# Performance work log

Measured on AMD Instinct MI355X. Metric: run time of the kernel, lower is better.

The kernel has to match this reference:

```python
import jax, jax.numpy as jnp
import numpy as np

B, S, I, H = 32, 1024, 512, 512


def setup_inputs() -> dict:
    key = jax.random.key(0)
    ks = jax.random.split(key, 5)
    scale_ih = 1.0 / np.sqrt(I)
    scale_hh = 1.0 / np.sqrt(H)
    return {
        "x": jax.random.normal(ks[0], (B, S, I), dtype=jnp.float32),
        "W_ih": jax.random.normal(ks[1], (4 * H, I), dtype=jnp.float32) * scale_ih,
        "W_hh": jax.random.normal(ks[2], (4 * H, H), dtype=jnp.float32) * scale_hh,
        "b_ih": jax.random.normal(ks[3], (4 * H,), dtype=jnp.float32) * scale_hh,
        "b_hh": jax.random.normal(ks[4], (4 * H,), dtype=jnp.float32) * scale_hh,
        "h0": jnp.zeros((B, H), dtype=jnp.float32),
        "c0": jnp.zeros((B, H), dtype=jnp.float32),
    }


def reference(x, W_ih, W_hh, b_ih, b_hh, h0, c0):
    # Precompute input contribution for all timesteps: [B, S, 4H]
    x_gates = jnp.einsum('bsi,gi->bsg', x, W_ih) + b_ih + b_hh

    def step(carry, xg_t):
        h, c = carry
        gates = xg_t + h @ W_hh.T  # [B, 4H]
        i_g, f_g, g_g, o_g = jnp.split(gates, 4, axis=-1)
        i_g = jax.nn.sigmoid(i_g)
        f_g = jax.nn.sigmoid(f_g)
        g_g = jnp.tanh(g_g)
        o_g = jax.nn.sigmoid(o_g)
        c_new = f_g * c + i_g * g_g
        h_new = o_g * jnp.tanh(c_new)
        return (h_new, c_new), h_new

    # scan over time: [S, B, 4H]
    (h_n, c_n), ys = jax.lax.scan(step, (h0, c0), jnp.swapaxes(x_gates, 0, 1))
    output = jnp.swapaxes(ys, 0, 1)  # [B, S, H]
    return output, h_n, c_n
```

## Files before the change

### kernel.cpp

```cpp
#include <hip/hip_runtime.h>
#include <stdint.h>


typedef __attribute__((ext_vector_type(8))) short bf16x8;
typedef __attribute__((ext_vector_type(4))) float f32x4;

__device__ __forceinline__ unsigned short f2bf(float f) {
  union { float f; unsigned u; } v; v.f = f;
  unsigned r = (v.u + 0x7fffu + ((v.u >> 16) & 1u)) >> 16;
  return (unsigned short)r;
}
__device__ __forceinline__ float bf2f(unsigned short h) {
  union { unsigned u; float f; } v; v.u = ((unsigned)h) << 16;
  return v.f;
}

__global__ __launch_bounds__(256) void cvt_bf16(const float* __restrict__ in,
                                                unsigned short* __restrict__ out, int n) {
  int i = (blockIdx.x * 256 + threadIdx.x) * 4;
  if (i >= n) return;
  float4 v = *(const float4*)(in + i);
  ushort4 o;
  o.x = f2bf(v.x); o.y = f2bf(v.y); o.z = f2bf(v.z); o.w = f2bf(v.w);
  *(ushort4*)(out + i) = o;
}

__global__ __launch_bounds__(256) void gemm_xg(const unsigned short* __restrict__ A,
                                               const unsigned short* __restrict__ Bw,
                                               const float* __restrict__ b_ih,
                                               const float* __restrict__ b_hh,
                                               unsigned short* __restrict__ xg) {
  __shared__ unsigned short Asub[128][32];
  __shared__ unsigned short Bsub[128][32];
  const int tid = threadIdx.x;
  const int mb = blockIdx.x >> 4;
  const int nb = blockIdx.x & 15;
  const int wv = tid >> 6, ln = tid & 63;
  const int wr = wv >> 1, wc = wv & 1;
  const int lrow = tid >> 1;
  const int lseg = (tid & 1) * 16;

  const unsigned short* Ag = A + (size_t)(mb * 128 + lrow) * 512 + lseg;
  const unsigned short* Bg = Bw + (size_t)(nb * 128 + lrow) * 512 + lseg;

  f32x4 acc[4][4] = {};
  const int frow = ln & 15;
  const int kq = (ln >> 4) * 8;

  for (int k0 = 0; k0 < 512; k0 += 32) {
    uint4 a0 = *(const uint4*)(Ag + k0);
    uint4 a1 = *(const uint4*)(Ag + k0 + 8);
    uint4 b0 = *(const uint4*)(Bg + k0);
    uint4 b1 = *(const uint4*)(Bg + k0 + 8);
    __syncthreads();
    *(uint4*)&Asub[lrow][lseg]     = a0;
    *(uint4*)&Asub[lrow][lseg + 8] = a1;
    *(uint4*)&Bsub[lrow][lseg]     = b0;
    *(uint4*)&Bsub[lrow][lseg + 8] = b1;
    __syncthreads();
    bf16x8 af[4], bfr[4];
#pragma unroll
    for (int mi = 0; mi < 4; ++mi)
      af[mi] = *(const bf16x8*)&Asub[wr * 64 + mi * 16 + frow][kq];
#pragma unroll
    for (int ni = 0; ni < 4; ++ni)
      bfr[ni] = *(const bf16x8*)&Bsub[wc * 64 + ni * 16 + frow][kq];
#pragma unroll
    for (int mi = 0; mi < 4; ++mi)
#pragma unroll
      for (int ni = 0; ni < 4; ++ni)
        acc[mi][ni] = __builtin_amdgcn_mfma_f32_16x16x32_bf16(af[mi], bfr[ni], acc[mi][ni], 0, 0, 0);
  }

  const int col0 = nb * 128 + wc * 64 + frow;
  float bias[4];
#pragma unroll
  for (int ni = 0; ni < 4; ++ni)
    bias[ni] = b_ih[col0 + ni * 16] + b_hh[col0 + ni * 16];

#pragma unroll
  for (int mi = 0; mi < 4; ++mi) {
    const int m0 = mb * 128 + wr * 64 + mi * 16 + (ln >> 4) * 4;
#pragma unroll
    for (int ni = 0; ni < 4; ++ni) {
#pragma unroll
      for (int rr = 0; rr < 4; ++rr) {
        float v = acc[mi][ni][rr] + bias[ni];
        xg[(size_t)(m0 + rr) * 2048 + col0 + ni * 16] = f2bf(v);
      }
    }
  }
}

__global__ __launch_bounds__(256, 1) void lstm_rec(const unsigned short* __restrict__ xg,
                                                   const float* __restrict__ W_hh,
                                                   const float* __restrict__ h0,
                                                   const float* __restrict__ c0,
                                                   float* __restrict__ out,
                                                   float* __restrict__ hn,
                                                   float* __restrict__ cn,
                                                   float* h_buf,
                                                   unsigned int* cnt) {
  __shared__ float h_lds[2048];
  __shared__ float scratch[64 * 17];
  __shared__ float gates_lds[64 * 5];
  __shared__ float c_lds[64];

  const int tid = threadIdx.x;
  const int g = blockIdx.x >> 5;
  const int w = blockIdx.x & 31;
  const int gb0 = g * 4;
  const int kc = tid >> 6;
  const int r = tid & 63;
  const int grow = (r >> 4) * 512 + w * 16 + (r & 15);
  const int kcb = kc * 128;
  unsigned int* my_cnt = cnt + g * 64;

  float W[128];
  {
    const float* wp = W_hh + (size_t)grow * 512 + kcb;
#pragma unroll
    for (int i = 0; i < 128; i += 4) {
      float4 v = *(const float4*)(wp + i);
      W[i] = v.x; W[i + 1] = v.y; W[i + 2] = v.z; W[i + 3] = v.w;
    }
  }
#pragma unroll
  for (int i = 0; i < 128; ++i) asm volatile("" : "+v"(W[i]));

  {
    const float* hp = h0 + gb0 * 512 + tid * 8;
    float4 va = *(const float4*)hp;
    float4 vb = *(const float4*)(hp + 4);
    *(float4*)&h_lds[tid * 8] = va;
    *(float4*)&h_lds[tid * 8 + 4] = vb;
    if (tid < 64) {
      int jj = tid & 15, bb = tid >> 4;
      c_lds[bb * 16 + jj] = c0[(gb0 + bb) * 512 + w * 16 + jj];
    }
  }
  __syncthreads();

  for (int t = 0; t < 1024; ++t) {
    float xg_v = bf2f(xg[(size_t)((gb0 + kc) * 1024 + t) * 2048 + grow]);

    float acc0 = 0.f, acc1 = 0.f, acc2 = 0.f, acc3 = 0.f;
#pragma unroll
    for (int i = 0; i < 128; i += 4) {
      float4 ha = *(const float4*)&h_lds[kcb + i];
      float4 hb = *(const float4*)&h_lds[512 + kcb + i];
      float4 hc = *(const float4*)&h_lds[1024 + kcb + i];
      float4 hd = *(const float4*)&h_lds[1536 + kcb + i];
      acc0 = fmaf(W[i], ha.x, acc0); acc0 = fmaf(W[i + 1], ha.y, acc0);
      acc0 = fmaf(W[i + 2], ha.z, acc0); acc0 = fmaf(W[i + 3], ha.w, acc0);
      acc1 = fmaf(W[i], hb.x, acc1); acc1 = fmaf(W[i + 1], hb.y, acc1);
      acc1 = fmaf(W[i + 2], hb.z, acc1); acc1 = fmaf(W[i + 3], hb.w, acc1);
      acc2 = fmaf(W[i], hc.x, acc2); acc2 = fmaf(W[i + 1], hc.y, acc2);
      acc2 = fmaf(W[i + 2], hc.z, acc2); acc2 = fmaf(W[i + 3], hc.w, acc2);
      acc3 = fmaf(W[i], hd.x, acc3); acc3 = fmaf(W[i + 1], hd.y, acc3);
      acc3 = fmaf(W[i + 2], hd.z, acc3); acc3 = fmaf(W[i + 3], hd.w, acc3);
    }
    scratch[r * 17 + kc] = acc0;
    scratch[r * 17 + 4 + kc] = acc1;
    scratch[r * 17 + 8 + kc] = acc2;
    scratch[r * 17 + 12 + kc] = acc3;
    __syncthreads();

    {
      float s = xg_v + scratch[r * 17 + kc * 4] + scratch[r * 17 + kc * 4 + 1]
                     + scratch[r * 17 + kc * 4 + 2] + scratch[r * 17 + kc * 4 + 3];
      gates_lds[r * 5 + kc] = s;
    }
    __syncthreads();

    if (tid < 64) {
      const int jj = tid & 15, bb = tid >> 4;
      float gi = gates_lds[jj * 5 + bb];
      float gf = gates_lds[(16 + jj) * 5 + bb];
      float gc = gates_lds[(32 + jj) * 5 + bb];
      float go = gates_lds[(48 + jj) * 5 + bb];
      float ig = 1.f / (1.f + __expf(-gi));
      float fg = 1.f / (1.f + __expf(-gf));
      float gt = tanhf(gc);
      float og = 1.f / (1.f + __expf(-go));
      float c = fmaf(fg, c_lds[bb * 16 + jj], ig * gt);
      c_lds[bb * 16 + jj] = c;
      float hv = og * tanhf(c);
      out[(size_t)((gb0 + bb) * 1024 + t) * 512 + w * 16 + jj] = hv;
      __hip_atomic_store(&h_buf[((t + 1) & 1) * 16384 + (gb0 + bb) * 512 + w * 16 + jj], hv,
                         __ATOMIC_RELAXED, __HIP_MEMORY_SCOPE_AGENT);
      if (t == 1023) {
        hn[(gb0 + bb) * 512 + w * 16 + jj] = hv;
        cn[(gb0 + bb) * 512 + w * 16 + jj] = c;
      }
    }
    __syncthreads();

    if (t < 1023) {
      if (tid == 0) {
        __hip_atomic_fetch_add(my_cnt, 1u, __ATOMIC_RELAXED, __HIP_MEMORY_SCOPE_AGENT);
        const unsigned target = 32u * (unsigned)(t + 1);
        while (__hip_atomic_load(my_cnt, __ATOMIC_RELAXED, __HIP_MEMORY_SCOPE_AGENT) < target)
          __builtin_amdgcn_s_sleep(2);
      }
      __syncthreads();
      const unsigned long long* hb =
          (const unsigned long long*)(h_buf + ((t + 1) & 1) * 16384 + gb0 * 512 + tid * 8);
      unsigned long long v[4];
#pragma unroll
      for (int q = 0; q < 4; ++q)
        v[q] = __hip_atomic_load(hb + q, __ATOMIC_RELAXED, __HIP_MEMORY_SCOPE_AGENT);
#pragma unroll
      for (int q = 0; q < 4; ++q)
        *(unsigned long long*)&h_lds[tid * 8 + q * 2] = v[q];
      __syncthreads();
    }
  }
}

extern "C" void kernel_launch(void* const* d_in, const int* in_sizes, int n_in,
                              void* d_out, int out_size, void* d_ws, size_t ws_size,
                              hipStream_t stream) {
  const float* x    = (const float*)d_in[0];
  const float* W_ih = (const float*)d_in[1];
  const float* W_hh = (const float*)d_in[2];
  const float* b_ih = (const float*)d_in[3];
  const float* b_hh = (const float*)d_in[4];
  const float* h0   = (const float*)d_in[5];
  const float* c0   = (const float*)d_in[6];
  float* out = (float*)d_out;
  float* hn = out + (size_t)32 * 1024 * 512;
  float* cn = hn + 32 * 512;

  uint8_t* ws = (uint8_t*)d_ws;
  unsigned short* xg   = (unsigned short*)ws;
  unsigned short* x_bf = (unsigned short*)(ws + 134217728u);
  unsigned short* w_bf = (unsigned short*)(ws + 167772160u);
  float* h_buf         = (float*)(ws + 169869312u);
  unsigned int* cnt    = (unsigned int*)(ws + 170000384u);

  hipMemsetAsync(cnt, 0, 8 * 256, stream);
  cvt_bf16<<<dim3(16384), dim3(256), 0, stream>>>(x, x_bf, 16777216);
  cvt_bf16<<<dim3(1024), dim3(256), 0, stream>>>(W_ih, w_bf, 1048576);
  gemm_xg<<<dim3(4096), dim3(256), 0, stream>>>(x_bf, w_bf, b_ih, b_hh, xg);

  void* args[] = {(void*)&xg, (void*)&W_hh, (void*)&h0, (void*)&c0,
                  (void*)&out, (void*)&hn, (void*)&cn, (void*)&h_buf, (void*)&cnt};
  hipLaunchCooperativeKernel((const void*)lstm_rec, dim3(256), dim3(256), args, 0, stream);
}
```

Baseline: 3.894 ms.

## Move W_hh to LDS and replace atomic counter barrier with per-block flags

Recurrent weights are staged into a padded LDS tile instead of being held in 128 registers per thread, and the inner dot-product reads them as float4 from LDS. The group barrier changes from a shared fetch-add counter to per-block step flags polled in parallel by one wavefront with a ballot. This frees registers and removes atomic contention on one counter, but adds LDS traffic per timestep and uses most of the LDS capacity.

```diff
diff --git a/kernel.cpp b/kernel.cpp
--- a/kernel.cpp
+++ b/kernel.cpp
@@ -92,15 +92,17 @@
   }
 }
 
-__global__ __launch_bounds__(256, 1) void lstm_rec(const unsigned short* __restrict__ xg,
-                                                   const float* __restrict__ W_hh,
-                                                   const float* __restrict__ h0,
-                                                   const float* __restrict__ c0,
-                                                   float* __restrict__ out,
-                                                   float* __restrict__ hn,
-                                                   float* __restrict__ cn,
-                                                   float* h_buf,
-                                                   unsigned int* cnt) {
+#define WSTRIDE 516
+__global__ __launch_bounds__(256) void lstm_rec(const unsigned short* __restrict__ xg,
+                                                const float* __restrict__ W_hh,
+                                                const float* __restrict__ h0,
+                                                const float* __restrict__ c0,
+                                                float* __restrict__ out,
+                                                float* __restrict__ hn,
+                                                float* __restrict__ cn,
+                                                float* h_buf,
+                                                unsigned int* flags) {
+  __shared__ float W_lds[64 * WSTRIDE];
   __shared__ float h_lds[2048];
   __shared__ float scratch[64 * 17];
   __shared__ float gates_lds[64 * 5];
@@ -112,21 +114,19 @@
   const int gb0 = g * 4;
   const int kc = tid >> 6;
   const int r = tid & 63;
-  const int grow = (r >> 4) * 512 + w * 16 + (r & 15);
   const int kcb = kc * 128;
-  unsigned int* my_cnt = cnt + g * 64;
-
-  float W[128];
-  {
-    const float* wp = W_hh + (size_t)grow * 512 + kcb;
-#pragma unroll
-    for (int i = 0; i < 128; i += 4) {
-      float4 v = *(const float4*)(wp + i);
-      W[i] = v.x; W[i + 1] = v.y; W[i + 2] = v.z; W[i + 3] = v.w;
-    }
-  }
-#pragma unroll
-  for (int i = 0; i < 128; ++i) asm volatile("" : "+v"(W[i]));
+  unsigned int* my_flags = flags + g * 64;
+
+#pragma unroll
+  for (int q = 0; q < 4; ++q) {
+    const float* src = W_hh + ((size_t)q * 512 + w * 16) * 512;
+    for (int u = tid * 4; u < 8192; u += 1024) {
+      float4 v = *(const float4*)(src + u);
+      int lr = q * 16 + (u >> 9);
+      int col = u & 511;
+      *(float4*)&W_lds[lr * WSTRIDE + col] = v;
+    }
+  }
 
   {
     const float* hp = h0 + gb0 * 512 + tid * 8;
@@ -141,24 +141,28 @@
   }
   __syncthreads();
 
+  const float* Wp = &W_lds[r * WSTRIDE + kcb];
+  const int grow = (r >> 4) * 512 + w * 16 + (r & 15);
+
   for (int t = 0; t < 1024; ++t) {
     float xg_v = bf2f(xg[(size_t)((gb0 + kc) * 1024 + t) * 2048 + grow]);
 
     float acc0 = 0.f, acc1 = 0.f, acc2 = 0.f, acc3 = 0.f;
 #pragma unroll
     for (int i = 0; i < 128; i += 4) {
+      float4 wv = *(const float4*)(Wp + i);
       float4 ha = *(const float4*)&h_lds[kcb + i];
       float4 hb = *(const float4*)&h_lds[512 + kcb + i];
       float4 hc = *(const float4*)&h_lds[1024 + kcb + i];
       float4 hd = *(const float4*)&h_lds[1536 + kcb + i];
-      acc0 = fmaf(W[i], ha.x, acc0); acc0 = fmaf(W[i + 1], ha.y, acc0);
-      acc0 = fmaf(W[i + 2], ha.z, acc0); acc0 = fmaf(W[i + 3], ha.w, acc0);
-      acc1 = fmaf(W[i], hb.x, acc1); acc1 = fmaf(W[i + 1], hb.y, acc1);
-      acc1 = fmaf(W[i + 2], hb.z, acc1); acc1 = fmaf(W[i + 3], hb.w, acc1);
-      acc2 = fmaf(W[i], hc.x, acc2); acc2 = fmaf(W[i + 1], hc.y, acc2);
-      acc2 = fmaf(W[i + 2], hc.z, acc2); acc2 = fmaf(W[i + 3], hc.w, acc2);
-      acc3 = fmaf(W[i], hd.x, acc3); acc3 = fmaf(W[i + 1], hd.y, acc3);
-      acc3 = fmaf(W[i + 2], hd.z, acc3); acc3 = fmaf(W[i + 3], hd.w, acc3);
+      acc0 = fmaf(wv.x, ha.x, acc0); acc0 = fmaf(wv.y, ha.y, acc0);
+      acc0 = fmaf(wv.z, ha.z, acc0); acc0 = fmaf(wv.w, ha.w, acc0);
+      acc1 = fmaf(wv.x, hb.x, acc1); acc1 = fmaf(wv.y, hb.y, acc1);
+      acc1 = fmaf(wv.z, hb.z, acc1); acc1 = fmaf(wv.w, hb.w, acc1);
+      acc2 = fmaf(wv.x, hc.x, acc2); acc2 = fmaf(wv.y, hc.y, acc2);
+      acc2 = fmaf(wv.z, hc.z, acc2); acc2 = fmaf(wv.w, hc.w, acc2);
+      acc3 = fmaf(wv.x, hd.x, acc3); acc3 = fmaf(wv.y, hd.y, acc3);
+      acc3 = fmaf(wv.z, hd.z, acc3); acc3 = fmaf(wv.w, hd.w, acc3);
     }
     scratch[r * 17 + kc] = acc0;
     scratch[r * 17 + 4 + kc] = acc1;
@@ -197,11 +201,16 @@
     __syncthreads();
 
     if (t < 1023) {
-      if (tid == 0) {
-        __hip_atomic_fetch_add(my_cnt, 1u, __ATOMIC_RELAXED, __HIP_MEMORY_SCOPE_AGENT);
-        const unsigned target = 32u * (unsigned)(t + 1);
-        while (__hip_atomic_load(my_cnt, __ATOMIC_RELAXED, __HIP_MEMORY_SCOPE_AGENT) < target)
-          __builtin_amdgcn_s_sleep(2);
+      if (tid == 0)
+        __hip_atomic_store(&my_flags[w], (unsigned)(t + 1),
+                           __ATOMIC_RELAXED, __HIP_MEMORY_SCOPE_AGENT);
+      if (tid < 32) {
+        for (;;) {
+          unsigned v = __hip_atomic_load(&my_flags[tid], __ATOMIC_RELAXED,
+                                         __HIP_MEMORY_SCOPE_AGENT);
+          if (__ballot(v > (unsigned)t) == 0xFFFFFFFFull) break;
+          __builtin_amdgcn_s_sleep(1);
+        }
       }
       __syncthreads();
       const unsigned long long* hb =
@@ -237,14 +246,14 @@
   unsigned short* x_bf = (unsigned short*)(ws + 134217728u);
   unsigned short* w_bf = (unsigned short*)(ws + 167772160u);
   float* h_buf         = (float*)(ws + 169869312u);
-  unsigned int* cnt    = (unsigned int*)(ws + 170000384u);
-
-  hipMemsetAsync(cnt, 0, 8 * 256, stream);
+  unsigned int* flags  = (unsigned int*)(ws + 170000384u);
+
+  hipMemsetAsync(flags, 0, 8 * 256, stream);
   cvt_bf16<<<dim3(16384), dim3(256), 0, stream>>>(x, x_bf, 16777216);
   cvt_bf16<<<dim3(1024), dim3(256), 0, stream>>>(W_ih, w_bf, 1048576);
   gemm_xg<<<dim3(4096), dim3(256), 0, stream>>>(x_bf, w_bf, b_ih, b_hh, xg);
 
   void* args[] = {(void*)&xg, (void*)&W_hh, (void*)&h0, (void*)&c0,
-                  (void*)&out, (void*)&hn, (void*)&cn, (void*)&h_buf, (void*)&cnt};
+                  (void*)&out, (void*)&hn, (void*)&cn, (void*)&h_buf, (void*)&flags};
   hipLaunchCooperativeKernel((const void*)lstm_rec, dim3(256), dim3(256), args, 0, stream);
 }
```

Result: slower. 4.191 ms (+7.6%).
